# Kernel optimization log

Measured on AMD Instinct MI355X. Metric: run time of the kernel, lower is better.

Reference implementation:

```python
import jax, jax.numpy as jnp
import numpy as np

NUM_CAPSULE = 10
DIM_CAPSULE = 16
ROUTINGS = 3
EPS = 1e-7  # K.epsilon()


def squash(x, axis=-1):
    # bojone squash: x / sqrt(s2 + eps) * s2 / (1 + s2)
    s2 = jnp.sum(jnp.square(x), axis=axis, keepdims=True)
    return x * s2 / ((1.0 + s2) * jnp.sqrt(s2 + EPS))


def setup_inputs() -> dict:
    key = jax.random.key(0)
    k1, k2 = jax.random.split(key)
    B, N, D_in = 64, 2048, 128  # batch, input_num_capsule, input_dim_capsule
    u_vecs = jax.random.normal(k1, (B, N, D_in), dtype=jnp.float32)
    fan_out = NUM_CAPSULE * DIM_CAPSULE
    limit = float(np.sqrt(6.0 / (D_in + fan_out)))  # glorot_uniform
    W = jax.random.uniform(k2, (D_in, fan_out), dtype=jnp.float32,
                           minval=-limit, maxval=limit)
    return {"u_vecs": u_vecs, "W": W}


def reference(u_vecs, W):
    B, N, _ = u_vecs.shape
    # share_weights=True: conv1d with kernel size 1 == matmul over feature dim
    u_hat = (u_vecs @ W).reshape(B, N, NUM_CAPSULE, DIM_CAPSULE)
    u_hat = jnp.transpose(u_hat, (0, 2, 1, 3))  # (B, J, N, D)
    b = jnp.zeros((B, NUM_CAPSULE, N), dtype=u_vecs.dtype)
    o = jnp.zeros((B, NUM_CAPSULE, DIM_CAPSULE), dtype=u_vecs.dtype)
    for i in range(ROUTINGS):
        c = jax.nn.softmax(b, axis=1)           # softmax over output capsules
        o = jnp.einsum('bjn,bjnd->bjd', c, u_hat)
        if i < ROUTINGS - 1:
            b = jnp.einsum('bjd,bjnd->bjn', o, u_hat)  # agreement update
    return squash(o)
```

## Files before the change

kernel.cpp:

```cpp
#include <hip/hip_runtime.h>
#include <math.h>


#define BATCH 64
#define NN    2048
#define KD    128
#define JCAP  10
#define DCAP  16
#define JDIM  160
#define EPSQ  1e-7f

__global__ __launch_bounds__(256) void k_colsum(const float* __restrict__ u,
                                                float* __restrict__ S) {
  const int b    = blockIdx.y;
  const int tile = blockIdx.x;
  const int t    = threadIdx.x;
  const int k4   = (t & 31) * 4;
  const int rg   = t >> 5;
  const float* p = u + ((size_t)(b * NN) + tile * 256 + rg * 32) * KD + k4;
  float a0 = 0.f, a1 = 0.f, a2 = 0.f, a3 = 0.f;
#pragma unroll 4
  for (int r = 0; r < 32; ++r) {
    float4 w = *(const float4*)(p + (size_t)r * KD);
    a0 += w.x; a1 += w.y; a2 += w.z; a3 += w.w;
  }
  atomicAdd(&S[b * KD + k4 + 0], a0);
  atomicAdd(&S[b * KD + k4 + 1], a1);
  atomicAdd(&S[b * KD + k4 + 2], a2);
  atomicAdd(&S[b * KD + k4 + 3], a3);
}

__global__ __launch_bounds__(256) void k_makeV(const float* __restrict__ Gin,
                                               const float* __restrict__ W,
                                               float* __restrict__ V,
                                               int fromS, float scale) {
  const int b = blockIdx.x;
  const int t = threadIdx.x;
  __shared__ float o_s[JDIM];
  if (t < JDIM) {
    const int j = t >> 4;
    const float* g = fromS ? (Gin + b * KD) : (Gin + (size_t)(b * JCAP + j) * KD);
    float acc = 0.f;
#pragma unroll 4
    for (int k = 0; k < KD; ++k) acc += g[k] * W[k * JDIM + t];
    o_s[t] = acc * scale;
  }
  __syncthreads();
  const int k = t & 127, gg = t >> 7;
#pragma unroll
  for (int i = 0; i < 5; ++i) {
    const int j = gg * 5 + i;
    const float* wp = W + k * JDIM + j * DCAP;
    float acc = 0.f;
#pragma unroll
    for (int d = 0; d < DCAP; ++d) acc += wp[d] * o_s[j * DCAP + d];
    V[(size_t)(b * JCAP + j) * KD + k] = acc;
  }
}

__global__ __launch_bounds__(256) void k_route(const float* __restrict__ u,
                                               const float* __restrict__ V,
                                               float* __restrict__ G) {
  const int b    = blockIdx.y;
  const int tile = blockIdx.x;
  const int t    = threadIdx.x;
  const int r0   = tile * 256;
  __shared__ float Cs[JCAP][260];
  __shared__ float Gp[4][JCAP][KD];

  {
    const float* up = u + (size_t)(b * NN + r0 + t) * KD;
    const float* vb = V + (size_t)(b * JCAP) * KD;
    float acc[JCAP];
#pragma unroll
    for (int j = 0; j < JCAP; ++j) acc[j] = 0.f;
    for (int kc = 0; kc < KD; kc += 8) {
      float4 xa = *(const float4*)(up + kc);
      float4 xb = *(const float4*)(up + kc + 4);
#pragma unroll
      for (int j = 0; j < JCAP; ++j) {
        const float4 v0 = *(const float4*)(vb + j * KD + kc);
        const float4 v1 = *(const float4*)(vb + j * KD + kc + 4);
        acc[j] += xa.x * v0.x + xa.y * v0.y + xa.z * v0.z + xa.w * v0.w
                + xb.x * v1.x + xb.y * v1.y + xb.z * v1.z + xb.w * v1.w;
      }
    }
    float m = acc[0];
#pragma unroll
    for (int j = 1; j < JCAP; ++j) m = fmaxf(m, acc[j]);
    float s = 0.f;
#pragma unroll
    for (int j = 0; j < JCAP; ++j) { acc[j] = __expf(acc[j] - m); s += acc[j]; }
    const float inv = 1.f / s;
#pragma unroll
    for (int j = 0; j < JCAP; ++j) Cs[j][t] = acc[j] * inv;
  }
  __syncthreads();

  {
    const int wave = t >> 6, lane = t & 63;
    const int rw = wave * 64;
    float g0[JCAP], g1[JCAP];
#pragma unroll
    for (int j = 0; j < JCAP; ++j) { g0[j] = 0.f; g1[j] = 0.f; }
    const float* ub = u + (size_t)(b * NN + r0 + rw) * KD + 2 * lane;
    for (int rc = 0; rc < 64; rc += 4) {
      float ua[4], ubv[4];
#pragma unroll
      for (int q = 0; q < 4; ++q) {
        float2 w = *(const float2*)(ub + (size_t)(rc + q) * KD);
        ua[q] = w.x; ubv[q] = w.y;
      }
#pragma unroll
      for (int j = 0; j < JCAP; ++j) {
        float4 c4 = *(const float4*)&Cs[j][rw + rc];
        g0[j] += c4.x * ua[0] + c4.y * ua[1] + c4.z * ua[2] + c4.w * ua[3];
        g1[j] += c4.x * ubv[0] + c4.y * ubv[1] + c4.z * ubv[2] + c4.w * ubv[3];
      }
    }
#pragma unroll
    for (int j = 0; j < JCAP; ++j) {
      *(float2*)&Gp[wave][j][2 * lane] = make_float2(g0[j], g1[j]);
    }
  }
  __syncthreads();

  for (int i = t; i < JCAP * KD; i += 256) {
    const int j = i >> 7, k = i & 127;
    float v = Gp[0][j][k] + Gp[1][j][k] + Gp[2][j][k] + Gp[3][j][k];
    atomicAdd(&G[(size_t)(b * JCAP + j) * KD + k], v);
  }
}

__global__ __launch_bounds__(256) void k_out(const float* __restrict__ G,
                                             const float* __restrict__ W,
                                             float* __restrict__ out) {
  const int b = blockIdx.x;
  const int t = threadIdx.x;
  __shared__ float o_s[JDIM];
  __shared__ float sc[JCAP];
  if (t < JDIM) {
    const int j = t >> 4;
    const float* g = G + (size_t)(b * JCAP + j) * KD;
    float acc = 0.f;
#pragma unroll 4
    for (int k = 0; k < KD; ++k) acc += g[k] * W[k * JDIM + t];
    o_s[t] = acc;
  }
  __syncthreads();
  if (t < JCAP) {
    float s2 = 0.f;
#pragma unroll
    for (int d = 0; d < DCAP; ++d) { float x = o_s[t * DCAP + d]; s2 += x * x; }
    sc[t] = s2 / ((1.f + s2) * sqrtf(s2 + EPSQ));
  }
  __syncthreads();
  if (t < JDIM) out[b * JDIM + t] = o_s[t] * sc[t >> 4];
}

extern "C" void kernel_launch(void* const* d_in, const int* in_sizes, int n_in,
                              void* d_out, int out_size, void* d_ws, size_t ws_size,
                              hipStream_t stream) {
  const float* u = (const float*)d_in[0];
  const float* W = (const float*)d_in[1];
  float* out = (float*)d_out;

  float* ws = (float*)d_ws;
  float* S  = ws;
  float* G1 = ws + 8192;
  float* G2 = ws + 8192 + 81920;
  float* V  = ws + 8192 + 2 * 81920;
  const size_t zero_bytes = (size_t)(8192 + 2 * 81920) * sizeof(float);
  hipMemsetAsync(d_ws, 0, zero_bytes, stream);

  k_colsum<<<dim3(8, BATCH), 256, 0, stream>>>(u, S);
  k_makeV <<<BATCH, 256, 0, stream>>>(S, W, V, 1, 0.1f);
  k_route <<<dim3(8, BATCH), 256, 0, stream>>>(u, V, G1);
  k_makeV <<<BATCH, 256, 0, stream>>>(G1, W, V, 0, 1.0f);
  k_route <<<dim3(8, BATCH), 256, 0, stream>>>(u, V, G2);
  k_out   <<<BATCH, 256, 0, stream>>>(G2, W, out);
}
```

Baseline: 183.1 us.

## Fuse capsule routing into one cooperative kernel with grid syncs

Replaces the memset and six kernel launches with a single cooperative kernel of 512 blocks. Grid-wide syncs separate the column-sum, routing and output phases, and each block recomputes its batch's V vectors into shared memory instead of reading them from a global buffer. The final W projection moves into the second routing pass and accumulates atomically into O2. A non-cooperative fallback path built on per-tile partial buffers (no atomics) is kept in case the cooperative launch fails. The trade-off is that launch overhead and gaps between kernels are swapped for grid-barrier costs, and occupancy is limited to 2 blocks per CU.

```diff
diff --git a/kernel.cpp b/kernel.cpp
--- a/kernel.cpp
+++ b/kernel.cpp
@@ -1,5 +1,8 @@
 #include <hip/hip_runtime.h>
+#include <hip/hip_cooperative_groups.h>
 #include <math.h>
+
+namespace cg = cooperative_groups;
 
 
 #define BATCH 64
@@ -9,41 +12,245 @@
 #define DCAP  16
 #define JDIM  160
 #define EPSQ  1e-7f
-
-__global__ __launch_bounds__(256) void k_colsum(const float* __restrict__ u,
-                                                float* __restrict__ S) {
-  const int b    = blockIdx.y;
-  const int tile = blockIdx.x;
+#define NBLK  512
+#define TPB   256
+
+__global__ __launch_bounds__(TPB, 2) void k_caps(const float* __restrict__ u,
+                                                 const float* __restrict__ W,
+                                                 float* __restrict__ out,
+                                                 float* __restrict__ ws) {
+  cg::grid_group grid = cg::this_grid();
+  const int g    = blockIdx.x;
   const int t    = threadIdx.x;
-  const int k4   = (t & 31) * 4;
-  const int rg   = t >> 5;
+  const int b    = g >> 3;
+  const int tile = g & 7;
+  const int r0   = tile * 256;
+
+  float* S  = ws;
+  float* G1 = ws + 8192;
+  float* O2 = ws + 8192 + 81920;
+
+  __shared__ __align__(16) float V_s[JCAP * KD];
+  __shared__ __align__(16) float Big[4 * JCAP * KD];
+  __shared__ float o_s[JDIM];
+  __shared__ float sc[JCAP];
+#define CS(j, r)     Big[(j) * 260 + (r)]
+#define GP(w, j, k)  Big[(w) * (JCAP * KD) + (j) * KD + (k)]
+
+  {
+    const int idx = g * TPB + t;
+    if (idx < 8192 + 81920 + 10240) ws[idx] = 0.f;
+  }
+  grid.sync();
+
+  {
+    const int k4 = (t & 31) * 4;
+    const int rg = t >> 5;
+    const float* p = u + ((size_t)(b * NN) + r0 + rg * 32) * KD + k4;
+    float4 a = make_float4(0.f, 0.f, 0.f, 0.f);
+#pragma unroll 4
+    for (int r = 0; r < 32; ++r) {
+      float4 w = *(const float4*)(p + (size_t)r * KD);
+      a.x += w.x; a.y += w.y; a.z += w.z; a.w += w.w;
+    }
+    float4* red = (float4*)Big;
+    red[t] = a;
+    __syncthreads();
+    if (t < 32) {
+      float4 s4 = red[t];
+#pragma unroll
+      for (int rg2 = 1; rg2 < 8; ++rg2) {
+        float4 w = red[rg2 * 32 + t];
+        s4.x += w.x; s4.y += w.y; s4.z += w.z; s4.w += w.w;
+      }
+      atomicAdd(&S[b * KD + t * 4 + 0], s4.x);
+      atomicAdd(&S[b * KD + t * 4 + 1], s4.y);
+      atomicAdd(&S[b * KD + t * 4 + 2], s4.z);
+      atomicAdd(&S[b * KD + t * 4 + 3], s4.w);
+    }
+  }
+  grid.sync();
+
+  for (int pass = 0; pass < 2; ++pass) {
+    {
+      if (t < JDIM) {
+        const int j = t >> 4;
+        const float* gs = pass == 0 ? (S + b * KD)
+                                    : (G1 + (size_t)(b * JCAP + j) * KD);
+        float acc = 0.f;
+#pragma unroll 4
+        for (int k = 0; k < KD; ++k) acc += gs[k] * W[k * JDIM + t];
+        o_s[t] = pass == 0 ? acc * 0.1f : acc;
+      }
+      __syncthreads();
+      const int k = t & 127, gg = t >> 7;
+#pragma unroll
+      for (int i = 0; i < 5; ++i) {
+        const int j = gg * 5 + i;
+        const float* wp = W + k * JDIM + j * DCAP;
+        float acc = 0.f;
+#pragma unroll
+        for (int d = 0; d < DCAP; ++d) acc += wp[d] * o_s[j * DCAP + d];
+        V_s[j * KD + k] = acc;
+      }
+      __syncthreads();
+    }
+
+    {
+      const float* up = u + (size_t)(b * NN + r0 + t) * KD;
+      float acc[JCAP];
+#pragma unroll
+      for (int j = 0; j < JCAP; ++j) acc[j] = 0.f;
+      for (int kc = 0; kc < KD; kc += 8) {
+        float4 xa = *(const float4*)(up + kc);
+        float4 xb = *(const float4*)(up + kc + 4);
+#pragma unroll
+        for (int j = 0; j < JCAP; ++j) {
+          float4 v0 = *(const float4*)(V_s + j * KD + kc);
+          float4 v1 = *(const float4*)(V_s + j * KD + kc + 4);
+          acc[j] += xa.x * v0.x + xa.y * v0.y + xa.z * v0.z + xa.w * v0.w
+                  + xb.x * v1.x + xb.y * v1.y + xb.z * v1.z + xb.w * v1.w;
+        }
+      }
+      float m = acc[0];
+#pragma unroll
+      for (int j = 1; j < JCAP; ++j) m = fmaxf(m, acc[j]);
+      float s = 0.f;
+#pragma unroll
+      for (int j = 0; j < JCAP; ++j) { acc[j] = __expf(acc[j] - m); s += acc[j]; }
+      const float inv = 1.f / s;
+#pragma unroll
+      for (int j = 0; j < JCAP; ++j) CS(j, t) = acc[j] * inv;
+    }
+    __syncthreads();
+
+    {
+      const int wave = t >> 6, lane = t & 63;
+      const int rw = wave * 64;
+      float g0[JCAP], g1[JCAP];
+#pragma unroll
+      for (int j = 0; j < JCAP; ++j) { g0[j] = 0.f; g1[j] = 0.f; }
+      const float* ub = u + (size_t)(b * NN + r0 + rw) * KD + 2 * lane;
+      for (int rc = 0; rc < 64; rc += 4) {
+        float ua[4], uc[4];
+#pragma unroll
+        for (int q = 0; q < 4; ++q) {
+          float2 w = *(const float2*)(ub + (size_t)(rc + q) * KD);
+          ua[q] = w.x; uc[q] = w.y;
+        }
+#pragma unroll
+        for (int j = 0; j < JCAP; ++j) {
+          float4 c4 = *(const float4*)&CS(j, rw + rc);
+          g0[j] += c4.x * ua[0] + c4.y * ua[1] + c4.z * ua[2] + c4.w * ua[3];
+          g1[j] += c4.x * uc[0] + c4.y * uc[1] + c4.z * uc[2] + c4.w * uc[3];
+        }
+      }
+      __syncthreads();
+#pragma unroll
+      for (int j = 0; j < JCAP; ++j)
+        *(float2*)&GP(wave, j, 2 * lane) = make_float2(g0[j], g1[j]);
+    }
+    __syncthreads();
+
+    if (pass == 0) {
+      for (int i = t; i < JCAP * KD; i += TPB) {
+        float v = GP(0, 0, i) + GP(1, 0, i) + GP(2, 0, i) + GP(3, 0, i);
+        atomicAdd(&G1[(size_t)b * JCAP * KD + i], v);
+      }
+      grid.sync();
+    } else {
+      for (int i = t; i < JCAP * KD; i += TPB)
+        GP(0, 0, i) = GP(0, 0, i) + GP(1, 0, i) + GP(2, 0, i) + GP(3, 0, i);
+      __syncthreads();
+      if (t < JDIM) {
+        const int j = t >> 4;
+        float acc = 0.f;
+#pragma unroll 4
+        for (int k = 0; k < KD; ++k) acc += GP(0, j, k) * W[k * JDIM + t];
+        atomicAdd(&O2[b * JDIM + t], acc);
+      }
+      grid.sync();
+    }
+  }
+
+  if (tile == 0) {
+    if (t < JDIM) o_s[t] = O2[b * JDIM + t];
+    __syncthreads();
+    if (t < JCAP) {
+      float s2 = 0.f;
+#pragma unroll
+      for (int d = 0; d < DCAP; ++d) { float x = o_s[t * DCAP + d]; s2 += x * x; }
+      sc[t] = s2 / ((1.f + s2) * sqrtf(s2 + EPSQ));
+    }
+    __syncthreads();
+    if (t < JDIM) out[b * JDIM + t] = o_s[t] * sc[t >> 4];
+  }
+#undef CS
+#undef GP
+}
+
+#define WS_SP   0
+#define WS_V    65536
+#define WS_GP1  147456
+#define WS_O2P  802816
+
+__global__ __launch_bounds__(TPB) void f_colsum(const float* __restrict__ u,
+                                                float* __restrict__ Sp) {
+  const int b = blockIdx.y, tile = blockIdx.x, t = threadIdx.x;
+  const int k4 = (t & 31) * 4, rg = t >> 5;
+  __shared__ float4 red[256];
   const float* p = u + ((size_t)(b * NN) + tile * 256 + rg * 32) * KD + k4;
-  float a0 = 0.f, a1 = 0.f, a2 = 0.f, a3 = 0.f;
+  float4 a = make_float4(0.f, 0.f, 0.f, 0.f);
 #pragma unroll 4
   for (int r = 0; r < 32; ++r) {
     float4 w = *(const float4*)(p + (size_t)r * KD);
-    a0 += w.x; a1 += w.y; a2 += w.z; a3 += w.w;
-  }
-  atomicAdd(&S[b * KD + k4 + 0], a0);
-  atomicAdd(&S[b * KD + k4 + 1], a1);
-  atomicAdd(&S[b * KD + k4 + 2], a2);
-  atomicAdd(&S[b * KD + k4 + 3], a3);
-}
-
-__global__ __launch_bounds__(256) void k_makeV(const float* __restrict__ Gin,
+    a.x += w.x; a.y += w.y; a.z += w.z; a.w += w.w;
+  }
+  red[t] = a;
+  __syncthreads();
+  if (t < 32) {
+    float4 s4 = red[t];
+#pragma unroll
+    for (int rg2 = 1; rg2 < 8; ++rg2) {
+      float4 w = red[rg2 * 32 + t];
+      s4.x += w.x; s4.y += w.y; s4.z += w.z; s4.w += w.w;
+    }
+    *(float4*)&Sp[(size_t)(b * 8 + tile) * KD + t * 4] = s4;
+  }
+}
+
+__global__ __launch_bounds__(TPB) void f_makeV(const float* __restrict__ ws,
                                                const float* __restrict__ W,
                                                float* __restrict__ V,
-                                               int fromS, float scale) {
-  const int b = blockIdx.x;
-  const int t = threadIdx.x;
+                                               int pass) {
+  const int b = blockIdx.x, t = threadIdx.x;
+  __shared__ float gsum[JCAP * KD];
   __shared__ float o_s[JDIM];
+  if (pass == 0) {
+    const float* Sp = ws + WS_SP + (size_t)b * 8 * KD;
+    if (t < KD) {
+      float s = 0.f;
+#pragma unroll
+      for (int tl = 0; tl < 8; ++tl) s += Sp[tl * KD + t];
+      gsum[t] = s * 0.1f;
+    }
+  } else {
+    const float* Gp1 = ws + WS_GP1 + (size_t)b * 8 * JCAP * KD;
+    for (int i = t; i < JCAP * KD; i += TPB) {
+      float s = 0.f;
+#pragma unroll
+      for (int tl = 0; tl < 8; ++tl) s += Gp1[tl * JCAP * KD + i];
+      gsum[i] = s;
+    }
+  }
+  __syncthreads();
   if (t < JDIM) {
     const int j = t >> 4;
-    const float* g = fromS ? (Gin + b * KD) : (Gin + (size_t)(b * JCAP + j) * KD);
+    const float* gs = pass == 0 ? gsum : (gsum + j * KD);
     float acc = 0.f;
 #pragma unroll 4
-    for (int k = 0; k < KD; ++k) acc += g[k] * W[k * JDIM + t];
-    o_s[t] = acc * scale;
+    for (int k = 0; k < KD; ++k) acc += gs[k] * W[k * JDIM + t];
+    o_s[t] = acc;
   }
   __syncthreads();
   const int k = t & 127, gg = t >> 7;
@@ -58,16 +265,15 @@
   }
 }
 
-__global__ __launch_bounds__(256) void k_route(const float* __restrict__ u,
+__global__ __launch_bounds__(TPB) void f_route(const float* __restrict__ u,
                                                const float* __restrict__ V,
-                                               float* __restrict__ G) {
-  const int b    = blockIdx.y;
-  const int tile = blockIdx.x;
-  const int t    = threadIdx.x;
-  const int r0   = tile * 256;
-  __shared__ float Cs[JCAP][260];
-  __shared__ float Gp[4][JCAP][KD];
-
+                                               const float* __restrict__ W,
+                                               float* __restrict__ dst,
+                                               int pass) {
+  const int b = blockIdx.y, tile = blockIdx.x, t = threadIdx.x;
+  const int r0 = tile * 256;
+  __shared__ __align__(16) float Cs[JCAP][260];
+  __shared__ __align__(16) float Gp[4][JCAP][KD];
   {
     const float* up = u + (size_t)(b * NN + r0 + t) * KD;
     const float* vb = V + (size_t)(b * JCAP) * KD;
@@ -79,8 +285,8 @@
       float4 xb = *(const float4*)(up + kc + 4);
 #pragma unroll
       for (int j = 0; j < JCAP; ++j) {
-        const float4 v0 = *(const float4*)(vb + j * KD + kc);
-        const float4 v1 = *(const float4*)(vb + j * KD + kc + 4);
+        float4 v0 = *(const float4*)(vb + j * KD + kc);
+        float4 v1 = *(const float4*)(vb + j * KD + kc + 4);
         acc[j] += xa.x * v0.x + xa.y * v0.y + xa.z * v0.z + xa.w * v0.w
                 + xb.x * v1.x + xb.y * v1.y + xb.z * v1.z + xb.w * v1.w;
       }
@@ -96,7 +302,6 @@
     for (int j = 0; j < JCAP; ++j) Cs[j][t] = acc[j] * inv;
   }
   __syncthreads();
-
   {
     const int wave = t >> 6, lane = t & 63;
     const int rw = wave * 64;
@@ -105,47 +310,53 @@
     for (int j = 0; j < JCAP; ++j) { g0[j] = 0.f; g1[j] = 0.f; }
     const float* ub = u + (size_t)(b * NN + r0 + rw) * KD + 2 * lane;
     for (int rc = 0; rc < 64; rc += 4) {
-      float ua[4], ubv[4];
+      float ua[4], uc[4];
 #pragma unroll
       for (int q = 0; q < 4; ++q) {
         float2 w = *(const float2*)(ub + (size_t)(rc + q) * KD);
-        ua[q] = w.x; ubv[q] = w.y;
+        ua[q] = w.x; uc[q] = w.y;
       }
 #pragma unroll
       for (int j = 0; j < JCAP; ++j) {
         float4 c4 = *(const float4*)&Cs[j][rw + rc];
         g0[j] += c4.x * ua[0] + c4.y * ua[1] + c4.z * ua[2] + c4.w * ua[3];
-        g1[j] += c4.x * ubv[0] + c4.y * ubv[1] + c4.z * ubv[2] + c4.w * ubv[3];
-      }
-    }
-#pragma unroll
-    for (int j = 0; j < JCAP; ++j) {
+        g1[j] += c4.x * uc[0] + c4.y * uc[1] + c4.z * uc[2] + c4.w * uc[3];
+      }
+    }
+#pragma unroll
+    for (int j = 0; j < JCAP; ++j)
       *(float2*)&Gp[wave][j][2 * lane] = make_float2(g0[j], g1[j]);
-    }
-  }
-  __syncthreads();
-
-  for (int i = t; i < JCAP * KD; i += 256) {
-    const int j = i >> 7, k = i & 127;
-    float v = Gp[0][j][k] + Gp[1][j][k] + Gp[2][j][k] + Gp[3][j][k];
-    atomicAdd(&G[(size_t)(b * JCAP + j) * KD + k], v);
-  }
-}
-
-__global__ __launch_bounds__(256) void k_out(const float* __restrict__ G,
-                                             const float* __restrict__ W,
-                                             float* __restrict__ out) {
-  const int b = blockIdx.x;
-  const int t = threadIdx.x;
+  }
+  __syncthreads();
+  if (pass == 0) {
+    float* Gp1 = dst + (size_t)(b * 8 + tile) * JCAP * KD;
+    for (int i = t; i < JCAP * KD; i += TPB)
+      Gp1[i] = Gp[0][0][i] + Gp[1][0][i] + Gp[2][0][i] + Gp[3][0][i];
+  } else {
+    for (int i = t; i < JCAP * KD; i += TPB)
+      Gp[0][0][i] = Gp[0][0][i] + Gp[1][0][i] + Gp[2][0][i] + Gp[3][0][i];
+    __syncthreads();
+    if (t < JDIM) {
+      const int j = t >> 4;
+      float acc = 0.f;
+#pragma unroll 4
+      for (int k = 0; k < KD; ++k) acc += Gp[0][j][k] * W[k * JDIM + t];
+      dst[(size_t)(b * 8 + tile) * JDIM + t] = acc;
+    }
+  }
+}
+
+__global__ __launch_bounds__(TPB) void f_squash(const float* __restrict__ O2p,
+                                                float* __restrict__ out) {
+  const int b = blockIdx.x, t = threadIdx.x;
   __shared__ float o_s[JDIM];
   __shared__ float sc[JCAP];
   if (t < JDIM) {
-    const int j = t >> 4;
-    const float* g = G + (size_t)(b * JCAP + j) * KD;
-    float acc = 0.f;
-#pragma unroll 4
-    for (int k = 0; k < KD; ++k) acc += g[k] * W[k * JDIM + t];
-    o_s[t] = acc;
+    const float* p = O2p + (size_t)b * 8 * JDIM;
+    float s = 0.f;
+#pragma unroll
+    for (int tl = 0; tl < 8; ++tl) s += p[tl * JDIM + t];
+    o_s[t] = s;
   }
   __syncthreads();
   if (t < JCAP) {
@@ -164,19 +375,21 @@
   const float* u = (const float*)d_in[0];
   const float* W = (const float*)d_in[1];
   float* out = (float*)d_out;
-
-  float* ws = (float*)d_ws;
-  float* S  = ws;
-  float* G1 = ws + 8192;
-  float* G2 = ws + 8192 + 81920;
-  float* V  = ws + 8192 + 2 * 81920;
-  const size_t zero_bytes = (size_t)(8192 + 2 * 81920) * sizeof(float);
-  hipMemsetAsync(d_ws, 0, zero_bytes, stream);
-
-  k_colsum<<<dim3(8, BATCH), 256, 0, stream>>>(u, S);
-  k_makeV <<<BATCH, 256, 0, stream>>>(S, W, V, 1, 0.1f);
-  k_route <<<dim3(8, BATCH), 256, 0, stream>>>(u, V, G1);
-  k_makeV <<<BATCH, 256, 0, stream>>>(G1, W, V, 0, 1.0f);
-  k_route <<<dim3(8, BATCH), 256, 0, stream>>>(u, V, G2);
-  k_out   <<<BATCH, 256, 0, stream>>>(G2, W, out);
-}
+  float* ws  = (float*)d_ws;
+
+  void* args[] = {(void*)&u, (void*)&W, (void*)&out, (void*)&ws};
+  hipError_t e = hipLaunchCooperativeKernel((const void*)k_caps, dim3(NBLK),
+                                            dim3(TPB), args, 0, stream);
+  if (e == hipSuccess) return;
+
+  float* Sp  = ws + WS_SP;
+  float* V   = ws + WS_V;
+  float* Gp1 = ws + WS_GP1;
+  float* O2p = ws + WS_O2P;
+  f_colsum<<<dim3(8, BATCH), TPB, 0, stream>>>(u, Sp);
+  f_makeV <<<BATCH, TPB, 0, stream>>>(ws, W, V, 0);
+  f_route <<<dim3(8, BATCH), TPB, 0, stream>>>(u, V, W, Gp1, 0);
+  f_makeV <<<BATCH, TPB, 0, stream>>>(ws, W, V, 1);
+  f_route <<<dim3(8, BATCH), TPB, 0, stream>>>(u, V, W, O2p, 1);
+  f_squash<<<BATCH, TPB, 0, stream>>>(O2p, out);
+}
```

Result: slower. 381.5 us (+108.3%).
